# Kernel optimization log

Hardware: AMD Instinct MI355X
Metric: run time of the kernel (lower is better)

Reference implementation:

```python
import jax, jax.numpy as jnp
import numpy as np

D_MODEL = 512
N_QUBITS = 10
N_LAYERS = 2
N_TOKENS = 16384
DIM = 2 ** N_QUBITS


def _rx(t):
    c = jnp.cos(t / 2) + 0j
    s = -1j * jnp.sin(t / 2)
    return jnp.stack([jnp.stack([c, s]), jnp.stack([s, c])]).astype(jnp.complex64)


def _ry(t):
    c = jnp.cos(t / 2) + 0j
    s = jnp.sin(t / 2) + 0j
    return jnp.stack([jnp.stack([c, -s]), jnp.stack([s, c])]).astype(jnp.complex64)


def _rz(t):
    z = jnp.zeros((), jnp.complex64)
    return jnp.stack([jnp.stack([jnp.exp(-1j * t / 2), z]),
                      jnp.stack([z, jnp.exp(1j * t / 2)])]).astype(jnp.complex64)


def _apply_1q(state, q, U, n):
    # state: [B, 2^n]; qubit 0 is the most significant bit
    B = state.shape[0]
    s = state.reshape(B, 2 ** q, 2, 2 ** (n - q - 1))
    s = jnp.einsum('ij,bajk->baik', U, s)
    return s.reshape(B, 2 ** n)


def _simulate(psi, rot, ent, n):
    # psi: [B, 2^n] complex64. rot: [L, n, 3]. ent: [L, n-1].
    L = rot.shape[0]
    idx = jnp.arange(2 ** n)
    for l in range(L):
        for q in range(n):
            psi = _apply_1q(psi, q, _rx(rot[l, q, 0]), n)
            psi = _apply_1q(psi, q, _ry(rot[l, q, 1]), n)
            psi = _apply_1q(psi, q, _rz(rot[l, q, 2]), n)
        for i in range(n - 1):  # nearest-neighbor parameterized CZ (controlled-phase)
            q1, q2 = i, i + 1
            both = (((idx >> (n - 1 - q1)) & 1) & ((idx >> (n - 1 - q2)) & 1)) == 1
            phase = jnp.where(both, jnp.exp(1j * ent[l, i].astype(jnp.complex64)),
                              jnp.ones((), jnp.complex64))
            psi = psi * phase
    return psi


def setup_inputs() -> dict:
    key = jax.random.key(0)
    ks = jax.random.split(key, 6)
    return {
        'x': jax.random.normal(ks[0], (N_TOKENS, D_MODEL), jnp.float32),
        'W_in': jax.random.normal(ks[1], (DIM, D_MODEL), jnp.float32) / np.sqrt(D_MODEL),
        'b_in': jnp.zeros((DIM,), jnp.float32),
        'W_out': jax.random.normal(ks[2], (D_MODEL, DIM), jnp.float32) / np.sqrt(DIM),
        'b_out': jnp.zeros((D_MODEL,), jnp.float32),
        'rot': jax.random.normal(ks[3], (N_LAYERS, N_QUBITS, 3), jnp.float32),
        'ent': jax.random.normal(ks[4], (N_LAYERS, N_QUBITS - 1), jnp.float32),
        'ln_w': jnp.ones((D_MODEL,), jnp.float32),
        'ln_b': jnp.zeros((D_MODEL,), jnp.float32),
    }


def reference(x, W_in, b_in, W_out, b_out, rot, ent, ln_w, ln_b):
    n = rot.shape[1]
    # input projection to 2^n amplitudes, then L2-normalize (F.normalize, eps=1e-12)
    xq = x @ W_in.T + b_in
    norm = jnp.maximum(jnp.linalg.norm(xq, axis=-1, keepdims=True), 1e-12)
    psi = (xq / norm).astype(jnp.complex64)
    psi = _simulate(psi, rot, ent, n)
    probs = (psi.real ** 2 + psi.imag ** 2).astype(x.dtype)  # |amp|^2
    out = probs @ W_out.T + b_out
    # LayerNorm(d_model), eps=1e-5
    mu = jnp.mean(out, axis=-1, keepdims=True)
    var = jnp.mean((out - mu) ** 2, axis=-1, keepdims=True)
    return (out - mu) / jnp.sqrt(var + 1e-5) * ln_w + ln_b
```

## Files before the change

### kernel.cpp

```cpp
#include <hip/hip_runtime.h>
#include <cstdint>

#define TOKENS 16384
#define DMODEL 512
#define DIM    1024
#define NQ     10
#define NL     2
#define BM     128
#define BN     128
#define BK     32

typedef __bf16 bf16x8 __attribute__((ext_vector_type(8)));
typedef float  f32x4  __attribute__((ext_vector_type(4)));
typedef unsigned short u16x8 __attribute__((ext_vector_type(8)));

__device__ __forceinline__ float b2f(unsigned short h) {
    union { unsigned u; float f; } v; v.u = ((unsigned)h) << 16; return v.f;
}
__device__ __forceinline__ unsigned short f2b(float f) {
    unsigned u = __builtin_bit_cast(unsigned, f);
    return (unsigned short)((u + 0x7FFFu + ((u >> 16) & 1u)) >> 16);
}
__device__ __forceinline__ float2 cmul(float2 a, float2 b) {
    return make_float2(a.x * b.x - a.y * b.y, a.x * b.y + a.y * b.x);
}
__device__ __forceinline__ float2 cadd(float2 a, float2 b) {
    return make_float2(a.x + b.x, a.y + b.y);
}
__device__ __forceinline__ void async_copy16(const void* g, void* l) {
    __builtin_amdgcn_global_load_lds((const __attribute__((address_space(1))) void*)g,
                                     (__attribute__((address_space(3))) void*)l, 16, 0, 0);
}

__global__ __launch_bounds__(256)
void prep_all_kernel(const float* __restrict__ x,  unsigned short* __restrict__ xb,
                     const float* __restrict__ w2, unsigned short* __restrict__ w2b,
                     const float* __restrict__ W_in, unsigned short* __restrict__ wtT,
                     const float* __restrict__ rot, const float* __restrict__ ent,
                     const float* __restrict__ bin,
                     unsigned short* __restrict__ U, float* __restrict__ b2) {
    const int bid = blockIdx.x;
    const int t = threadIdx.x;

    if (bid < 256) {
        __shared__ float2 Gs[NL * NQ * 4];
        const int lane = t & 63;
        const int c = bid * 4 + (t >> 6);

        if (t < NL * NQ) {
            float tx = rot[t * 3 + 0] * 0.5f;
            float ty = rot[t * 3 + 1] * 0.5f;
            float tz = rot[t * 3 + 2] * 0.5f;
            float cx = cosf(tx), sx = sinf(tx);
            float cy = cosf(ty), sy = sinf(ty);
            float cz = cosf(tz), sz = sinf(tz);
            float2 rx00 = make_float2(cx, 0.f),  rx01 = make_float2(0.f, -sx);
            float2 rx10 = make_float2(0.f, -sx), rx11 = make_float2(cx, 0.f);
            float2 ry00 = make_float2(cy, 0.f),  ry01 = make_float2(-sy, 0.f);
            float2 ry10 = make_float2(sy, 0.f),  ry11 = make_float2(cy, 0.f);
            float2 m00 = cadd(cmul(ry00, rx00), cmul(ry01, rx10));
            float2 m01 = cadd(cmul(ry00, rx01), cmul(ry01, rx11));
            float2 m10 = cadd(cmul(ry10, rx00), cmul(ry11, rx10));
            float2 m11 = cadd(cmul(ry10, rx01), cmul(ry11, rx11));
            float2 e0 = make_float2(cz, -sz), e1 = make_float2(cz, sz);
            Gs[t * 4 + 0] = cmul(e0, m00);
            Gs[t * 4 + 1] = cmul(e0, m01);
            Gs[t * 4 + 2] = cmul(e1, m10);
            Gs[t * 4 + 3] = cmul(e1, m11);
        }
        float ef[NL * (NQ - 1)];
        #pragma unroll
        for (int i = 0; i < NL * (NQ - 1); i++) ef[i] = ent[i];
        __syncthreads();

        float2 amp[16];
        #pragma unroll
        for (int r = 0; r < 16; r++)
            amp[r] = make_float2((lane * 16 + r == c) ? 1.f : 0.f, 0.f);

        #pragma unroll 1
        for (int li = 0; li < NL; li++) {
            const int l = NL - 1 - li;
            #pragma unroll
            for (int r = 0; r < 16; r++) {
                int idx = lane * 16 + r;
                float ang = 0.f;
                #pragma unroll
                for (int q = 0; q < NQ - 1; q++) {
                    int both = ((idx >> (9 - q)) & 1) & ((idx >> (8 - q)) & 1);
                    if (both) ang += ef[l * (NQ - 1) + q];
                }
                amp[r] = cmul(amp[r], make_float2(cosf(ang), sinf(ang)));
            }
            const float2* Gl = Gs + l * NQ * 4;
            #pragma unroll
            for (int qq = 0; qq < NQ; qq++) {
                const int q = 9 - qq;
                float2 u00 = Gl[q * 4 + 0], u10 = Gl[q * 4 + 1];
                float2 u01 = Gl[q * 4 + 2], u11 = Gl[q * 4 + 3];
                if (q >= 6) {
                    const int S = 1 << (9 - q);
                    #pragma unroll
                    for (int r = 0; r < 16; r++) {
                        if (r & S) continue;
                        float2 a = amp[r], b = amp[r + S];
                        float2 n0, n1;
                        n0.x = u00.x * a.x - u00.y * a.y + u01.x * b.x - u01.y * b.y;
                        n0.y = u00.x * a.y + u00.y * a.x + u01.x * b.y + u01.y * b.x;
                        n1.x = u10.x * a.x - u10.y * a.y + u11.x * b.x - u11.y * b.y;
                        n1.y = u10.x * a.y + u10.y * a.x + u11.x * b.y + u11.y * b.x;
                        amp[r] = n0; amp[r + S] = n1;
                    }
                } else {
                    const int mask = 32 >> q;
                    int bit = (lane >> (5 - q)) & 1;
                    float2 ua = bit ? u11 : u00;
                    float2 ub = bit ? u10 : u01;
                    #pragma unroll
                    for (int r = 0; r < 16; r++) {
                        float px = __shfl_xor(amp[r].x, mask, 64);
                        float py = __shfl_xor(amp[r].y, mask, 64);
                        float nx = ua.x * amp[r].x - ua.y * amp[r].y + ub.x * px - ub.y * py;
                        float ny = ua.x * amp[r].y + ua.y * amp[r].x + ub.x * py + ub.y * px;
                        amp[r] = make_float2(nx, ny);
                    }
                }
            }
        }

        float accRe = 0.f, accIm = 0.f;
        #pragma unroll
        for (int i = 0; i < 4; i++) {
            float4 bv = *(const float4*)&bin[lane * 16 + i * 4];
            accRe += amp[i * 4 + 0].x * bv.x + amp[i * 4 + 1].x * bv.y
                   + amp[i * 4 + 2].x * bv.z + amp[i * 4 + 3].x * bv.w;
            accIm += amp[i * 4 + 0].y * bv.x + amp[i * 4 + 1].y * bv.y
                   + amp[i * 4 + 2].y * bv.z + amp[i * 4 + 3].y * bv.w;
        }
        #pragma unroll
        for (int m = 1; m < 64; m <<= 1) {
            accRe += __shfl_xor(accRe, m, 64);
            accIm += __shfl_xor(accIm, m, 64);
        }
        const int nR = ((c >> 5) << 6) + ((c & 1) << 5) + ((c >> 1) & 15);
        if (lane == 0) { b2[nR] = accRe; b2[nR + 16] = accIm; }

        u16x8 o0, o1, p0, p1;
        #pragma unroll
        for (int r = 0; r < 8; r++) {
            o0[r] = f2b(amp[r].x);     o1[r] = f2b(amp[r + 8].x);
            p0[r] = f2b(amp[r].y);     p1[r] = f2b(amp[r + 8].y);
        }
        unsigned short* rowRe = U + (size_t)nR * DIM + lane * 16;
        unsigned short* rowIm = U + (size_t)(nR + 16) * DIM + lane * 16;
        *(u16x8*)rowRe = o0; *(u16x8*)(rowRe + 8) = o1;
        *(u16x8*)rowIm = p0; *(u16x8*)(rowIm + 8) = p1;
        return;
    }

    if (bid < 768) {
        __shared__ float tile[32][33];
        const int b2i = bid - 256;
        const int tx = t & 31, ty = t >> 5;
        const int d0 = (b2i & 15) * 32, j0 = (b2i >> 4) * 32;
        #pragma unroll
        for (int i = 0; i < 32; i += 8)
            tile[ty + i][tx] = W_in[(size_t)(j0 + ty + i) * DMODEL + d0 + tx];
        __syncthreads();
        #pragma unroll
        for (int i = 0; i < 32; i += 8)
            wtT[(size_t)(d0 + ty + i) * DIM + j0 + tx] = f2b(tile[tx][ty + i]);
        return;
    }

    const int NX4 = TOKENS * DMODEL / 4;
    const int NW4 = DMODEL * DIM / 4;
    const int total = NX4 + NW4;
    const int stride = 2048 * 256;
    for (int i = (bid - 768) * 256 + t; i < total; i += stride) {
        const float* s; unsigned short* d; int j;
        if (i < NX4) { s = x;  d = xb;  j = i; }
        else         { s = w2; d = w2b; j = i - NX4; }
        float4 v = *(const float4*)&s[(size_t)j * 4];
        ushort4 o;
        o.x = f2b(v.x); o.y = f2b(v.y); o.z = f2b(v.z); o.w = f2b(v.w);
        *(ushort4*)&d[(size_t)j * 4] = o;
    }
}

__global__ __launch_bounds__(256)
void fold_kernel(const unsigned short* __restrict__ A, const unsigned short* __restrict__ B,
                 unsigned short* __restrict__ C) {
    __shared__ unsigned short sm[2 * 8192];
    const int t = threadIdx.x;
    const int wave = t >> 6, lane = t & 63;
    const int wm = wave >> 1, wn = wave & 1;
    const int laneR = lane & 15;
    const int bm0 = blockIdx.y * 64;
    const int bn0 = blockIdx.x * 64;

    const int csrc = (t & 7) ^ ((t >> 3) & 7);
    const int rowg = t >> 3;
    const unsigned aOff0 = (unsigned)(bm0 + rowg) * DIM + csrc * 8;
    const unsigned aOff1 = (unsigned)(bm0 + 32 + rowg) * DIM + csrc * 8;
    const unsigned bOff0 = (unsigned)(bn0 + rowg) * DIM + csrc * 8;
    const unsigned bOff1 = (unsigned)(bn0 + 32 + rowg) * DIM + csrc * 8;

    f32x4 acc[2][2] = {};

    #define F_STAGE(nbuf, kt) {                                            \
        unsigned short* d = sm + (nbuf) * 8192 + t * 8;                    \
        async_copy16(A + aOff0 + (kt) * 64, d);                            \
        async_copy16(A + aOff1 + (kt) * 64, d + 2048);                     \
        async_copy16(B + bOff0 + (kt) * 64, d + 4096);                     \
        async_copy16(B + bOff1 + (kt) * 64, d + 6144);                     \
    }

    F_STAGE(0, 0);
    asm volatile("s_waitcnt vmcnt(0)" ::: "memory");
    __syncthreads();

    #pragma unroll
    for (int kt = 0; kt < 16; kt++) {
        const int cur = kt & 1;
        if (kt < 15) F_STAGE(cur ^ 1, kt + 1);
        const unsigned short* la = sm + cur * 8192;
        const unsigned short* lb = la + 4096;
        #pragma unroll
        for (int kk = 0; kk < 2; kk++) {
            bf16x8 af[2], bfr[2];
            #pragma unroll
            for (int i = 0; i < 2; i++) {
                int row = wm * 32 + i * 16 + laneR;
                int slot = ((lane >> 4) + kk * 4) ^ (row & 7);
                af[i] = *(const bf16x8*)&la[row * 64 + slot * 8];
                int nrow = wn * 32 + i * 16 + laneR;
                int nslot = ((lane >> 4) + kk * 4) ^ (nrow & 7);
                bfr[i] = *(const bf16x8*)&lb[nrow * 64 + nslot * 8];
            }
            #pragma unroll
            for (int i = 0; i < 2; i++)
                #pragma unroll
                for (int j = 0; j < 2; j++)
                    acc[i][j] = __builtin_amdgcn_mfma_f32_16x16x32_bf16(af[i], bfr[j], acc[i][j], 0, 0, 0);
        }
        asm volatile("s_waitcnt vmcnt(0)" ::: "memory");
        __syncthreads();
    }
    #undef F_STAGE

    #pragma unroll
    for (int i = 0; i < 2; i++)
        #pragma unroll
        for (int j = 0; j < 2; j++) {
            int col = bn0 + wn * 32 + j * 16 + laneR;
            #pragma unroll
            for (int r = 0; r < 4; r++) {
                int row = bm0 + wm * 32 + i * 16 + (lane >> 4) * 4 + r;
                C[(size_t)row * DMODEL + col] = f2b(acc[i][j][r]);
            }
        }
}

__global__ __launch_bounds__(512, 2)
void gemm1_kernel(const unsigned short* __restrict__ A, const unsigned short* __restrict__ B,
                  const float* __restrict__ bias, unsigned short* __restrict__ P) {
    const int K = DMODEL;
    __shared__ unsigned short sm[2 * 32768];
    const int t = threadIdx.x;
    const int wave = t >> 6, lane = t & 63;
    const int wm = wave >> 2, wn = wave & 3;
    const int laneR = lane & 15;

    const int bid = blockIdx.x;
    const int swz = (bid & 7) * 64 + (bid >> 3);
    const int bm0 = (swz >> 3) * 256;
    const int bn0 = (swz & 7) * 256;

    const int csrc = (t & 3) ^ ((t >> 3) & 3);
    const int rowg = t >> 2;
    const unsigned aOff0 = (unsigned)(bm0 + rowg) * DMODEL + csrc * 8;
    const unsigned aOff1 = (unsigned)(bm0 + 128 + rowg) * DMODEL + csrc * 8;
    const unsigned bOff0 = (unsigned)(bn0 + rowg) * DMODEL + csrc * 8;
    const unsigned bOff1 = (unsigned)(bn0 + 128 + rowg) * DMODEL + csrc * 8;

    const int slotc = (((lane >> 4) ^ ((lane >> 1) & 3)) & 3) * 8;

    f32x4 acc[8][4] = {};

    #define G1_STAGE(nbuf, kk, kb)                                                 \
    {                                                                              \
        unsigned short* d0 = sm + (nbuf) * 32768 + (kk) * 8192 + wave * 512;       \
        async_copy16(A + aOff0 + (kb) + (kk) * 32, d0);                            \
        async_copy16(A + aOff1 + (kb) + (kk) * 32, d0 + 4096);                     \
        async_copy16(B + bOff0 + (kb) + (kk) * 32, d0 + 16384);                    \
        async_copy16(B + bOff1 + (kb) + (kk) * 32, d0 + 20480);                    \
    }

    #define G1_COMPUTE(cbuf, kk)                                                   \
    {                                                                              \
        const unsigned short* la = sm + (cbuf) * 32768 + (kk) * 8192;              \
        const unsigned short* lb = la + 16384;                                     \
        bf16x8 af[8], bfr[4];                                                      \
        _Pragma("unroll")                                                          \
        for (int i = 0; i < 8; i++)                                                \
            af[i] = *(const bf16x8*)&la[(wm * 128 + i * 16 + laneR) * 32 + slotc]; \
        _Pragma("unroll")                                                          \
        for (int j = 0; j < 4; j++)                                                \
            bfr[j] = *(const bf16x8*)&lb[(wn * 64 + j * 16 + laneR) * 32 + slotc]; \
        __builtin_amdgcn_s_setprio(1);                                             \
        _Pragma("unroll")                                                          \
        for (int i = 0; i < 8; i++)                                                \
            _Pragma("unroll")                                                      \
            for (int j = 0; j < 4; j++)                                            \
                acc[i][j] = __builtin_amdgcn_mfma_f32_16x16x32_bf16(af[i], bfr[j], acc[i][j], 0, 0, 0); \
        __builtin_amdgcn_s_setprio(0);                                             \
    }

    G1_STAGE(0, 0, 0);
    G1_STAGE(0, 1, 0);
    asm volatile("s_waitcnt vmcnt(4)" ::: "memory");
    asm volatile("s_barrier" ::: "memory");

    #pragma unroll
    for (int kt = 0; kt < 7; kt++) {
        const int cur = kt & 1, nxt = cur ^ 1;
        const unsigned kb = (unsigned)(kt + 1) * 64;
        G1_STAGE(nxt, 0, kb);
        G1_COMPUTE(cur, 0);
        asm volatile("s_waitcnt vmcnt(4)" ::: "memory");
        asm volatile("s_barrier" ::: "memory");
        G1_STAGE(nxt, 1, kb);
        G1_COMPUTE(cur, 1);
        asm volatile("s_waitcnt vmcnt(4)" ::: "memory");
        asm volatile("s_barrier" ::: "memory");
    }
    G1_COMPUTE(1, 0);
    asm volatile("s_waitcnt vmcnt(0)" ::: "memory");
    asm volatile("s_barrier" ::: "memory");
    G1_COMPUTE(1, 1);

    #undef G1_STAGE
    #undef G1_COMPUTE

    const int cb0 = bn0 + wn * 64 + laneR;
    const float b0 = bias[cb0];
    const float b1 = bias[cb0 + 16];
    const float b2v = bias[cb0 + 32];
    const float b3 = bias[cb0 + 48];
    const int pc2 = (bn0 >> 1) + wn * 32 + laneR * 2;
    #pragma unroll
    for (int i = 0; i < 8; i++) {
        #pragma unroll
        for (int r = 0; r < 4; r++) {
            int row = bm0 + wm * 128 + i * 16 + (lane >> 4) * 4 + r;
            float v0 = acc[i][0][r] + b0, v1 = acc[i][1][r] + b1;
            float v2 = acc[i][2][r] + b2v, v3 = acc[i][3][r] + b3;
            ushort2 o;
            o.x = f2b(v0 * v0 + v1 * v1);
            o.y = f2b(v2 * v2 + v3 * v3);
            *(ushort2*)&P[(size_t)row * DIM + pc2] = o;
        }
    }
}

__global__ __launch_bounds__(512)
void gemm2_ln_kernel(const unsigned short* __restrict__ A,
                     const unsigned short* __restrict__ B,
                     const float* __restrict__ bias,
                     const float* __restrict__ lw, const float* __restrict__ lb,
                     float* __restrict__ out) {
    __shared__ unsigned short sm[2 * 36864];
    __shared__ float redS[4][64], redQ[4][64];
    __shared__ float muS[64], rsS[64], n2s[64], n2p[4][64];
    const int t = threadIdx.x, wave = t >> 6, lane = t & 63;
    const int wm = wave >> 2, wn = wave & 3;
    const int laneR = lane & 15;
    const int bm0 = blockIdx.x * 64;

    const int csrc = (t & 3) ^ ((t >> 3) & 3);
    const int akk  = t >> 8, arow = (t >> 2) & 63;
    const unsigned aSrc = (unsigned)(bm0 + arow) * DIM + akk * 32 + csrc * 8;
    const int brow = t >> 2;
    const int slotc = (((lane >> 4) ^ ((lane >> 1) & 3)) & 3) * 8;

    f32x4 acc[2][8] = {};
    f32x4 accN[2] = {};
    bf16x8 ones;
    #pragma unroll
    for (int r = 0; r < 8; r++) ones[r] = (__bf16)1.0f;

    #define G2_STAGE_A(nbuf, kb) {                                          \
        async_copy16(A + aSrc + (kb), sm + (nbuf) * 36864 + t * 8);         \
    }
    #define G2_STAGE_B(nbuf, kk, kb) {                                      \
        unsigned short* d = sm + (nbuf) * 36864 + 4096 + (kk) * 16384 + t * 8; \
        const unsigned short* s0 = B + (size_t)brow * DIM + (kb) + (kk) * 32 + csrc * 8; \
        async_copy16(s0,                 d);                                 \
        async_copy16(s0 + 128 * DIM,     d + 4096);                         \
        async_copy16(s0 + 256 * DIM,     d + 8192);                         \
        async_copy16(s0 + 384 * DIM,     d + 12288);                        \
    }
    #define G2_COMPUTE(cbuf, kk, sel) {                                     \
        const unsigned short* la  = sm + (cbuf) * 36864 + (kk) * 2048;      \
        const unsigned short* lbp = sm + (cbuf) * 36864 + 4096 + (kk) * 16384; \
        bf16x8 af[2], bfr[8];                                               \
        _Pragma("unroll")                                                   \
        for (int i = 0; i < 2; i++)                                         \
            af[i] = *(const bf16x8*)&la[(wm * 32 + i * 16 + laneR) * 32 + slotc]; \
        _Pragma("unroll")                                                   \
        for (int j = 0; j < 8; j++)                                         \
            bfr[j] = *(const bf16x8*)&lbp[(wn * 128 + j * 16 + laneR) * 32 + slotc]; \
        __builtin_amdgcn_s_setprio(1);                                      \
        _Pragma("unroll")                                                   \
        for (int i = 0; i < 2; i++)                                         \
            _Pragma("unroll")                                               \
            for (int j = 0; j < 8; j++)                                     \
                acc[i][j] = __builtin_amdgcn_mfma_f32_16x16x32_bf16(af[i], bfr[j], acc[i][j], 0, 0, 0); \
        if (wn == (sel)) {                                                  \
            _Pragma("unroll")                                               \
            for (int i = 0; i < 2; i++)                                     \
                accN[i] = __builtin_amdgcn_mfma_f32_16x16x32_bf16(af[i], ones, accN[i], 0, 0, 0); \
        }                                                                   \
        __builtin_amdgcn_s_setprio(0);                                      \
    }

    G2_STAGE_A(0, 0); G2_STAGE_B(0, 0, 0); G2_STAGE_B(0, 1, 0);
    asm volatile("s_waitcnt vmcnt(4)" ::: "memory");
    asm volatile("s_barrier" ::: "memory");

    #pragma unroll
    for (int n = 0; n < 15; n++) {
        const int cb = n & 1, nb = cb ^ 1;
        const unsigned kb = (unsigned)(n + 1) * 64;
        G2_STAGE_A(nb, kb); G2_STAGE_B(nb, 0, kb);
        G2_COMPUTE(cb, 0, n & 3);
        asm volatile("s_waitcnt vmcnt(5)" ::: "memory");
        asm volatile("s_barrier" ::: "memory");
        G2_STAGE_B(nb, 1, kb);
        G2_COMPUTE(cb, 1, n & 3);
        asm volatile("s_waitcnt vmcnt(4)" ::: "memory");
        asm volatile("s_barrier" ::: "memory");
    }
    G2_COMPUTE(1, 0, 3);
    asm volatile("s_waitcnt vmcnt(0)" ::: "memory");
    asm volatile("s_barrier" ::: "memory");
    G2_COMPUTE(1, 1, 3);

    #undef G2_STAGE_A
    #undef G2_STAGE_B
    #undef G2_COMPUTE

    if (laneR == 0) {
        #pragma unroll
        for (int i = 0; i < 2; i++)
            #pragma unroll
            for (int r = 0; r < 4; r++)
                n2p[wn][wm * 32 + i * 16 + (lane >> 4) * 4 + r] = accN[i][r];
    }
    __syncthreads();
    if (t < 64)
        n2s[t] = n2p[0][t] + n2p[1][t] + n2p[2][t] + n2p[3][t];
    __syncthreads();

    float bvj[8];
    #pragma unroll
    for (int j = 0; j < 8; j++) bvj[j] = bias[wn * 128 + j * 16 + laneR];

    #pragma unroll
    for (int i = 0; i < 2; i++)
        #pragma unroll
        for (int r = 0; r < 4; r++) {
            int rl = wm * 32 + i * 16 + (lane >> 4) * 4 + r;
            float nn = 1.0f / fmaxf(n2s[rl], 1e-24f);
            float s = 0.f, q = 0.f;
            #pragma unroll
            for (int j = 0; j < 8; j++) {
                float val = acc[i][j][r] * nn + bvj[j];
                acc[i][j][r] = val;
                s += val; q += val * val;
            }
            s += __shfl_xor(s, 1, 64); q += __shfl_xor(q, 1, 64);
            s += __shfl_xor(s, 2, 64); q += __shfl_xor(q, 2, 64);
            s += __shfl_xor(s, 4, 64); q += __shfl_xor(q, 4, 64);
            s += __shfl_xor(s, 8, 64); q += __shfl_xor(q, 8, 64);
            if (laneR == 0) { redS[wn][rl] = s; redQ[wn][rl] = q; }
        }
    __syncthreads();
    if (t < 64) {
        float s = redS[0][t] + redS[1][t] + redS[2][t] + redS[3][t];
        float q = redQ[0][t] + redQ[1][t] + redQ[2][t] + redQ[3][t];
        float mu = s * (1.0f / DMODEL);
        float var = q * (1.0f / DMODEL) - mu * mu;
        muS[t] = mu;
        rsS[t] = rsqrtf(var + 1e-5f);
    }
    __syncthreads();
    #pragma unroll
    for (int i = 0; i < 2; i++)
        #pragma unroll
        for (int j = 0; j < 8; j++) {
            int col = wn * 128 + j * 16 + laneR;
            float w = lw[col], bb = lb[col];
            #pragma unroll
            for (int r = 0; r < 4; r++) {
                int rl = wm * 32 + i * 16 + (lane >> 4) * 4 + r;
                out[(size_t)(bm0 + rl) * DMODEL + col] =
                    (acc[i][j][r] - muS[rl]) * rsS[rl] * w + bb;
            }
        }
}

extern "C" void kernel_launch(void* const* d_in, const int* in_sizes, int n_in,
                              void* d_out, int out_size, void* d_ws, size_t ws_size,
                              hipStream_t stream) {
    (void)in_sizes; (void)n_in; (void)out_size; (void)ws_size;
    const float* x     = (const float*)d_in[0];
    const float* W_in  = (const float*)d_in[1];
    const float* b_in  = (const float*)d_in[2];
    const float* W_out = (const float*)d_in[3];
    const float* b_out = (const float*)d_in[4];
    const float* rot   = (const float*)d_in[5];
    const float* ent   = (const float*)d_in[6];
    const float* ln_w  = (const float*)d_in[7];
    const float* ln_b  = (const float*)d_in[8];
    float* out = (float*)d_out;

    char* ws = (char*)d_ws;
    unsigned short* p    = (unsigned short*)ws;
    unsigned short* x_bf = (unsigned short*)(ws + 33554432ull);
    unsigned short* wtT  = (unsigned short*)(ws + 50331648ull);
    unsigned short* w2b  = (unsigned short*)(ws + 51380224ull);
    unsigned short* Ucat = (unsigned short*)(ws + 52428800ull);
    unsigned short* W1c  = (unsigned short*)(ws + 56623104ull);
    float*          b2   = (float*)(ws + 58720256ull);

    prep_all_kernel<<<2816, 256, 0, stream>>>(x, x_bf, W_out, w2b, W_in, wtT,
                                              rot, ent, b_in, Ucat, b2);
    fold_kernel<<<dim3(DMODEL / 64, 2 * DIM / 64), 256, 0, stream>>>(Ucat, wtT, W1c);
    gemm1_kernel<<<512, 512, 0, stream>>>(x_bf, W1c, b2, p);
    gemm2_ln_kernel<<<TOKENS / 64, 512, 0, stream>>>(
        p, w2b, b_out, ln_w, ln_b, out);
}
```

Baseline: 196.7 us.

## Shrink gemm1 tile to 256x128 with single-K32 stages for higher occupancy

Changes the first GEMM from 256x256 tiles with 64-wide K steps to 256x128 tiles with 32-wide K steps, doubling the grid to 1024 blocks. LDS use drops and launch bounds ask for 4 blocks per CU, and the accumulator count halves to cut register pressure. Each block now stages only one K-half per buffer and waits on vmcnt(0) every step, which removes the partial-wait overlap. The epilogue writes single bf16 outputs instead of pairs, and B tiles are reloaded across more blocks.

```diff
diff --git a/kernel.cpp b/kernel.cpp
--- a/kernel.cpp
+++ b/kernel.cpp
@@ -6,9 +6,6 @@
 #define DIM    1024
 #define NQ     10
 #define NL     2
-#define BM     128
-#define BN     128
-#define BK     32
 
 typedef __bf16 bf16x8 __attribute__((ext_vector_type(8)));
 typedef float  f32x4  __attribute__((ext_vector_type(4)));
@@ -262,104 +259,87 @@
         }
 }
 
-__global__ __launch_bounds__(512, 2)
+__global__ __launch_bounds__(512, 4)
 void gemm1_kernel(const unsigned short* __restrict__ A, const unsigned short* __restrict__ B,
                   const float* __restrict__ bias, unsigned short* __restrict__ P) {
-    const int K = DMODEL;
-    __shared__ unsigned short sm[2 * 32768];
+    __shared__ unsigned short sm[2 * 12288];
     const int t = threadIdx.x;
     const int wave = t >> 6, lane = t & 63;
     const int wm = wave >> 2, wn = wave & 3;
     const int laneR = lane & 15;
 
     const int bid = blockIdx.x;
-    const int swz = (bid & 7) * 64 + (bid >> 3);
-    const int bm0 = (swz >> 3) * 256;
-    const int bn0 = (swz & 7) * 256;
+    const int swz = (bid & 7) * 128 + (bid >> 3);
+    const int bm0 = (swz >> 4) * 256;
+    const int bn0 = (swz & 15) * 128;
 
     const int csrc = (t & 3) ^ ((t >> 3) & 3);
     const int rowg = t >> 2;
     const unsigned aOff0 = (unsigned)(bm0 + rowg) * DMODEL + csrc * 8;
     const unsigned aOff1 = (unsigned)(bm0 + 128 + rowg) * DMODEL + csrc * 8;
     const unsigned bOff0 = (unsigned)(bn0 + rowg) * DMODEL + csrc * 8;
-    const unsigned bOff1 = (unsigned)(bn0 + 128 + rowg) * DMODEL + csrc * 8;
 
     const int slotc = (((lane >> 4) ^ ((lane >> 1) & 3)) & 3) * 8;
 
-    f32x4 acc[8][4] = {};
-
-    #define G1_STAGE(nbuf, kk, kb)                                                 \
+    f32x4 acc[8][2] = {};
+
+    #define G1_STAGE(nbuf, kb)                                                     \
     {                                                                              \
-        unsigned short* d0 = sm + (nbuf) * 32768 + (kk) * 8192 + wave * 512;       \
-        async_copy16(A + aOff0 + (kb) + (kk) * 32, d0);                            \
-        async_copy16(A + aOff1 + (kb) + (kk) * 32, d0 + 4096);                     \
-        async_copy16(B + bOff0 + (kb) + (kk) * 32, d0 + 16384);                    \
-        async_copy16(B + bOff1 + (kb) + (kk) * 32, d0 + 20480);                    \
-    }
-
-    #define G1_COMPUTE(cbuf, kk)                                                   \
+        unsigned short* d0 = sm + (nbuf) * 12288 + wave * 512;                     \
+        async_copy16(A + aOff0 + (kb), d0);                                        \
+        async_copy16(A + aOff1 + (kb), d0 + 4096);                                 \
+        async_copy16(B + bOff0 + (kb), d0 + 8192);                                 \
+    }
+
+    #define G1_COMPUTE(cbuf)                                                       \
     {                                                                              \
-        const unsigned short* la = sm + (cbuf) * 32768 + (kk) * 8192;              \
-        const unsigned short* lb = la + 16384;                                     \
-        bf16x8 af[8], bfr[4];                                                      \
+        const unsigned short* la = sm + (cbuf) * 12288;                            \
+        const unsigned short* lb = la + 8192;                                      \
+        bf16x8 af[8], bfr[2];                                                      \
         _Pragma("unroll")                                                          \
         for (int i = 0; i < 8; i++)                                                \
             af[i] = *(const bf16x8*)&la[(wm * 128 + i * 16 + laneR) * 32 + slotc]; \
         _Pragma("unroll")                                                          \
-        for (int j = 0; j < 4; j++)                                                \
-            bfr[j] = *(const bf16x8*)&lb[(wn * 64 + j * 16 + laneR) * 32 + slotc]; \
+        for (int j = 0; j < 2; j++)                                                \
+            bfr[j] = *(const bf16x8*)&lb[(wn * 32 + j * 16 + laneR) * 32 + slotc]; \
         __builtin_amdgcn_s_setprio(1);                                             \
         _Pragma("unroll")                                                          \
         for (int i = 0; i < 8; i++)                                                \
             _Pragma("unroll")                                                      \
-            for (int j = 0; j < 4; j++)                                            \
+            for (int j = 0; j < 2; j++)                                            \
                 acc[i][j] = __builtin_amdgcn_mfma_f32_16x16x32_bf16(af[i], bfr[j], acc[i][j], 0, 0, 0); \
         __builtin_amdgcn_s_setprio(0);                                             \
     }
 
-    G1_STAGE(0, 0, 0);
-    G1_STAGE(0, 1, 0);
-    asm volatile("s_waitcnt vmcnt(4)" ::: "memory");
-    asm volatile("s_barrier" ::: "memory");
-
-    #pragma unroll
-    for (int kt = 0; kt < 7; kt++) {
-        const int cur = kt & 1, nxt = cur ^ 1;
-        const unsigned kb = (unsigned)(kt + 1) * 64;
-        G1_STAGE(nxt, 0, kb);
-        G1_COMPUTE(cur, 0);
-        asm volatile("s_waitcnt vmcnt(4)" ::: "memory");
-        asm volatile("s_barrier" ::: "memory");
-        G1_STAGE(nxt, 1, kb);
-        G1_COMPUTE(cur, 1);
-        asm volatile("s_waitcnt vmcnt(4)" ::: "memory");
-        asm volatile("s_barrier" ::: "memory");
-    }
-    G1_COMPUTE(1, 0);
+    G1_STAGE(0, 0);
     asm volatile("s_waitcnt vmcnt(0)" ::: "memory");
     asm volatile("s_barrier" ::: "memory");
-    G1_COMPUTE(1, 1);
+
+    #pragma unroll
+    for (int kt = 0; kt < 16; kt++) {
+        const int cur = kt & 1;
+        if (kt < 15) G1_STAGE(cur ^ 1, (unsigned)(kt + 1) * 32);
+        G1_COMPUTE(cur);
+        asm volatile("s_waitcnt vmcnt(0)" ::: "memory");
+        asm volatile("s_barrier" ::: "memory");
+    }
 
     #undef G1_STAGE
     #undef G1_COMPUTE
 
-    const int cb0 = bn0 + wn * 64 + laneR;
-    const float b0 = bias[cb0];
-    const float b1 = bias[cb0 + 16];
-    const float b2v = bias[cb0 + 32];
-    const float b3 = bias[cb0 + 48];
-    const int pc2 = (bn0 >> 1) + wn * 32 + laneR * 2;
+    const int g64 = wn >> 1, bsel = wn & 1;
+    const int colRe = bn0 + g64 * 64 + bsel * 32 + laneR;
+    const float bRe = bias[colRe];
+    const float bIm = bias[colRe + 16];
+    const int pc = (bn0 >> 1) + g64 * 32 + laneR * 2 + bsel;
     #pragma unroll
     for (int i = 0; i < 8; i++) {
         #pragma unroll
         for (int r = 0; r < 4; r++) {
             int row = bm0 + wm * 128 + i * 16 + (lane >> 4) * 4 + r;
-            float v0 = acc[i][0][r] + b0, v1 = acc[i][1][r] + b1;
-            float v2 = acc[i][2][r] + b2v, v3 = acc[i][3][r] + b3;
-            ushort2 o;
-            o.x = f2b(v0 * v0 + v1 * v1);
-            o.y = f2b(v2 * v2 + v3 * v3);
-            *(ushort2*)&P[(size_t)row * DIM + pc2] = o;
+            float vr = acc[i][0][r] + bRe;
+            float vi = acc[i][1][r] + bIm;
+            P[(size_t)row * DIM + pc] = f2b(vr * vr + vi * vi);
         }
     }
 }
@@ -538,7 +518,7 @@
     prep_all_kernel<<<2816, 256, 0, stream>>>(x, x_bf, W_out, w2b, W_in, wtT,
                                               rot, ent, b_in, Ucat, b2);
     fold_kernel<<<dim3(DMODEL / 64, 2 * DIM / 64), 256, 0, stream>>>(Ucat, wtT, W1c);
-    gemm1_kernel<<<512, 512, 0, stream>>>(x_bf, W1c, b2, p);
+    gemm1_kernel<<<1024, 512, 0, stream>>>(x_bf, W1c, b2, p);
     gemm2_ln_kernel<<<TOKENS / 64, 512, 0, stream>>>(
         p, w2b, b_out, ln_w, ln_b, out);
 }
```

New measurement: 195.4 us. Within noise of the previous version (-0.7%).
